# Optimization experiments

Hardware: AMD Instinct MI355X
Metric: run time of the kernel (lower is better)

## Reference

```python
import jax, jax.numpy as jnp
import numpy as np

B, LMAX, T_OUT, VOCAB, EMB, CVEC, HID, OUT = 8192, 12, 10, 36, 300, 256, 256, 512


def setup_inputs() -> dict:
    key = jax.random.key(0)
    ks = jax.random.split(key, 16)
    s = lambda fan: 1.0 / np.sqrt(fan)
    u = lambda k, shape, b: jax.random.uniform(k, shape, jnp.float32, -b, b)
    inp = {
        'words': jax.random.randint(ks[0], (B, LMAX), 0, VOCAB),
        'lengths': 1 + jax.random.randint(ks[1], (B,), 0, LMAX),  # in [1, LMAX]
        'emb_table': jax.random.normal(ks[2], (VOCAB, EMB), jnp.float32),
        'enc_w': u(ks[3], (CVEC, EMB), s(EMB)),
        'enc_b': u(ks[4], (CVEC,), s(EMB)),
        'wih_f': u(ks[5], (4 * HID, CVEC), s(HID)),
        'whh_f': u(ks[6], (4 * HID, HID), s(HID)),
        'bih_f': u(ks[7], (4 * HID,), s(HID)),
        'bhh_f': u(ks[8], (4 * HID,), s(HID)),
        'wih_b': u(ks[9], (4 * HID, CVEC), s(HID)),
        'whh_b': u(ks[10], (4 * HID, HID), s(HID)),
        'bih_b': u(ks[11], (4 * HID,), s(HID)),
        'bhh_b': u(ks[12], (4 * HID,), s(HID)),
        'out_w': u(ks[13], (OUT, 2 * HID), s(2 * HID)),
        'out_b': u(ks[14], (OUT,), s(2 * HID)),
    }
    return inp


def _interp_words(emb_table, words, lengths):
    # bilinear resize (L,300)->(10,300) with align_corners=True; width unchanged
    # so it is exact linear interpolation along the char axis.
    def one(word_row, L):
        Lf = (L - 1).astype(jnp.float32)
        pos = jnp.arange(T_OUT, dtype=jnp.float32) * Lf / (T_OUT - 1)  # (10,)
        i0 = jnp.floor(pos).astype(jnp.int32)
        i1 = jnp.minimum(i0 + 1, L - 1).astype(jnp.int32)
        f = (pos - i0.astype(jnp.float32))[:, None]
        e = emb_table[word_row]  # (LMAX, EMB)
        return e[i0] * (1.0 - f) + e[i1] * f  # (10, EMB)
    return jax.vmap(one)(words, lengths)  # (B, 10, EMB)


def _lstm(seq, wih, whh, bih, bhh):
    # seq: (T, B, In); PyTorch gate order i, f, g, o
    bsz = seq.shape[1]
    h0 = jnp.zeros((bsz, HID), seq.dtype)
    c0 = jnp.zeros((bsz, HID), seq.dtype)

    def step(carry, x_t):
        h, c = carry
        g = x_t @ wih.T + h @ whh.T + (bih + bhh)
        i, f, gg, o = jnp.split(g, 4, axis=-1)
        c = jax.nn.sigmoid(f) * c + jax.nn.sigmoid(i) * jnp.tanh(gg)
        h = jax.nn.sigmoid(o) * jnp.tanh(c)
        return (h, c), h

    _, hs = jax.lax.scan(step, (h0, c0), seq)
    return hs  # (T, B, HID)


def reference(words, lengths, emb_table, enc_w, enc_b, wih_f, whh_f, bih_f, bhh_f,
              wih_b, whh_b, bih_b, bhh_b, out_w, out_b):
    emb = _interp_words(emb_table, words, lengths)              # (B, 10, 300)
    cv = jax.nn.relu(emb @ enc_w.T + enc_b)                     # (B, 10, 256)
    seq = jnp.transpose(cv, (1, 0, 2))                          # (10, B, 256)
    h_f = _lstm(seq, wih_f, whh_f, bih_f, bhh_f)                # (10, B, 256)
    h_b = _lstm(seq[::-1], wih_b, whh_b, bih_b, bhh_b)[::-1]    # (10, B, 256)
    rec = jnp.concatenate([h_f, h_b], axis=-1)                  # (10, B, 512)
    out = rec @ out_w.T + out_b                                 # (10, B, 512)
    return jnp.transpose(out, (1, 0, 2))                        # (B, 10, 512)
```

## Files before the change

### kernel.cpp

```cpp
#include <hip/hip_runtime.h>
#include <hip/hip_fp16.h>

typedef _Float16 f16;
typedef _Float16 f16x8 __attribute__((ext_vector_type(8)));
typedef float    f32x4 __attribute__((ext_vector_type(4)));

#define NB   8192
#define TOUT 10
#define LMAX 12
#define EMB  300

__device__ __forceinline__ float sigm_(float x) {
    return __builtin_amdgcn_rcpf(1.0f + __builtin_amdgcn_exp2f(x * -1.44269504f));
}
__device__ __forceinline__ float tanh_(float x) {
    return 1.0f - 2.0f * __builtin_amdgcn_rcpf(1.0f + __builtin_amdgcn_exp2f(x * 2.88539008f));
}

__global__ __launch_bounds__(256) void pack_w2(
    const float* __restrict__ wih_f, const float* __restrict__ whh_f,
    const float* __restrict__ wih_b, const float* __restrict__ whh_b,
    f16* __restrict__ Wp) {
    int idx = blockIdx.x * 256 + threadIdx.x;
    int d   = idx >> 19;
    int r   = idx & 524287;
    int tile = r >> 9;
    int e    = r & 511;
    int kc = tile >> 6, nt = tile & 63;
    int khi = e >> 7, rem = e & 127, nl = rem >> 3, klo = rem & 7;
    int n = nt * 16 + nl;
    int k = kc * 32 + khi * 8 + klo;
    int w = n >> 7, rr = n & 127, gate = rr >> 5, u = w * 32 + (rr & 31);
    int srow = gate * 256 + u;
    const float* wih = d ? wih_b : wih_f;
    const float* whh = d ? whh_b : whh_f;
    float v = (k < 256) ? wih[srow * 256 + k] : whh[srow * 256 + (k - 256)];
    Wp[idx] = (f16)v;
}

__global__ __launch_bounds__(256) void pack_bias(
    const float* __restrict__ bih_f, const float* __restrict__ bhh_f,
    const float* __restrict__ bih_b, const float* __restrict__ bhh_b,
    float* __restrict__ bp) {
    int idx = blockIdx.x * 256 + threadIdx.x;
    int d = idx >> 10, n = idx & 1023;
    int w = n >> 7, rr = n & 127, gate = rr >> 5, u = w * 32 + (rr & 31);
    int srow = gate * 256 + u;
    bp[idx] = d ? (bih_b[srow] + bhh_b[srow]) : (bih_f[srow] + bhh_f[srow]);
}

__global__ __launch_bounds__(256) void pack_w3(
    const float* __restrict__ out_w, f16* __restrict__ W3p) {
    int idx = blockIdx.x * 256 + threadIdx.x;
    int tile = idx >> 9, e = idx & 511;
    int kc = tile >> 5, nt = tile & 31;
    int khi = e >> 7, rem = e & 127, nl = rem >> 3, klo = rem & 7;
    int n = nt * 16 + nl, k = kc * 32 + khi * 8 + klo;
    W3p[idx] = (f16)out_w[n * 512 + k];
}

__global__ __launch_bounds__(256) void enc_proj(
    const float* __restrict__ tab, const float* __restrict__ ew,
    const float* __restrict__ eb, float* __restrict__ P) {
    int v = blockIdx.x, j = threadIdx.x;
    const float* a = tab + v * EMB;
    const float* w = ew + j * EMB;
    float s = 0.0f;
    for (int k = 0; k < EMB; ++k) s += a[k] * w[k];
    P[v * 256 + j] = s + eb[j];
}

__global__ __launch_bounds__(256) void build_seq(
    const int* __restrict__ words, const int* __restrict__ lengths,
    const float* __restrict__ P, f16* __restrict__ seqp) {
    int gi = blockIdx.x * 256 + threadIdx.x;
    int bl  = gi & 15;
    int khi = (gi >> 4) & 3;
    int kc  = (gi >> 6) & 7;
    int mt  = (gi >> 9) & 511;
    int t   = gi >> 18;
    int b = mt * 16 + bl;
    int L = lengths[b];
    float pos = ((float)t * (float)(L - 1)) / 9.0f;
    int i0 = (int)pos;
    float f = pos - (float)i0;
    int i1 = min(i0 + 1, L - 1);
    int c0 = words[b * LMAX + i0];
    int c1 = words[b * LMAX + i1];
    const float* p0 = P + c0 * 256 + kc * 32 + khi * 8;
    const float* p1 = P + c1 * 256 + kc * 32 + khi * 8;
    f16x8 r;
#pragma unroll
    for (int j = 0; j < 8; ++j) {
        float v = p0[j] * (1.0f - f) + p1[j] * f;
        v = fmaxf(v, 0.0f);
        r[j] = (f16)v;
    }
    *((f16x8*)seqp + gi) = r;
}

__global__ __launch_bounds__(512) void lstm_fused(
    const f16* __restrict__ seqp, const f16* __restrict__ Wp,
    const float* __restrict__ bp, f16* __restrict__ hcat) {
    const int dir  = blockIdx.x >> 7;
    const int r0t  = (blockIdx.x & 127) << 2;
    const int wave = threadIdx.x >> 6;
    const int lane = threadIdx.x & 63;
    const int l16  = lane & 15;
    const int quad = lane >> 4;

    __shared__ __align__(16) f16 hbuf[4 * 8 * 512];

    {
        f16x8 z = {(f16)0, (f16)0, (f16)0, (f16)0, (f16)0, (f16)0, (f16)0, (f16)0};
        for (int i = threadIdx.x; i < 2048; i += 512) ((f16x8*)hbuf)[i] = z;
    }

    const float* bpd = bp + dir * 1024 + wave * 128;
    float bias_l[8];
#pragma unroll
    for (int nt = 0; nt < 8; ++nt) bias_l[nt] = bpd[nt * 16 + l16];

    const f16* Wd = Wp + dir * 524288;

    float cst[4][4][2];
#pragma unroll
    for (int m = 0; m < 4; ++m)
#pragma unroll
        for (int q = 0; q < 4; ++q) { cst[m][q][0] = 0.0f; cst[m][q][1] = 0.0f; }

    __syncthreads();

    for (int step = 0; step < TOUT; ++step) {
        const int t = dir ? (9 - step) : step;
        f32x4 acc[4][8];
#pragma unroll
        for (int m = 0; m < 4; ++m)
#pragma unroll
            for (int nt = 0; nt < 8; ++nt)
#pragma unroll
                for (int q = 0; q < 4; ++q) acc[m][nt][q] = bias_l[nt];

        const f16* seqt = seqp + (size_t)(t * 512 + r0t) * 8 * 512;

#pragma unroll 2
        for (int kc = 0; kc < 8; ++kc) {
            f16x8 bfrag[8];
#pragma unroll
            for (int nt = 0; nt < 8; ++nt)
                bfrag[nt] = *(const f16x8*)(Wd + ((kc * 64 + wave * 8 + nt) * 512 + lane * 8));
            f16x8 afrag[4];
#pragma unroll
            for (int m = 0; m < 4; ++m)
                afrag[m] = *(const f16x8*)(seqt + ((m * 8 + kc) * 512 + lane * 8));
#pragma unroll
            for (int m = 0; m < 4; ++m)
#pragma unroll
                for (int nt = 0; nt < 8; ++nt)
                    acc[m][nt] = __builtin_amdgcn_mfma_f32_16x16x32_f16(
                        afrag[m], bfrag[nt], acc[m][nt], 0, 0, 0);
        }
#pragma unroll 2
        for (int kcl = 0; kcl < 8; ++kcl) {
            int kc = kcl + 8;
            f16x8 bfrag[8];
#pragma unroll
            for (int nt = 0; nt < 8; ++nt)
                bfrag[nt] = *(const f16x8*)(Wd + ((kc * 64 + wave * 8 + nt) * 512 + lane * 8));
            f16x8 afrag[4];
#pragma unroll
            for (int m = 0; m < 4; ++m)
                afrag[m] = *(const f16x8*)(hbuf + ((m * 8 + kcl) * 512 + lane * 8));
#pragma unroll
            for (int m = 0; m < 4; ++m)
#pragma unroll
                for (int nt = 0; nt < 8; ++nt)
                    acc[m][nt] = __builtin_amdgcn_mfma_f32_16x16x32_f16(
                        afrag[m], bfrag[nt], acc[m][nt], 0, 0, 0);
        }

        __syncthreads();

#pragma unroll
        for (int m = 0; m < 4; ++m) {
#pragma unroll
            for (int us = 0; us < 2; ++us) {
#pragma unroll
                for (int q = 0; q < 4; ++q) {
                    float gi_ = acc[m][0 + us][q];
                    float gf_ = acc[m][2 + us][q];
                    float gg_ = acc[m][4 + us][q];
                    float go_ = acc[m][6 + us][q];
                    float ii = sigm_(gi_), ff = sigm_(gf_);
                    float gg = tanh_(gg_), oo = sigm_(go_);
                    float c = ff * cst[m][q][us] + ii * gg;
                    cst[m][q][us] = c;
                    float h = oo * tanh_(c);
                    int u   = us * 16 + l16;
                    int row = quad * 4 + q;
                    hbuf[(m * 8 + wave) * 512 + ((u >> 3) * 16 + row) * 8 + (u & 7)] = (f16)h;
                }
            }
        }

        __syncthreads();

        for (int i = threadIdx.x; i < 2048; i += 512) {
            int off = i * 8;
            int m  = off >> 12;
            int kc = (off >> 9) & 7;
            int e  = off & 511;
            f16x8 v = *(const f16x8*)(hbuf + off);
            *(f16x8*)(hcat + ((size_t)((t * 512 + r0t + m) * 16 + dir * 8 + kc) * 512 + e)) = v;
        }
    }
}

__global__ __launch_bounds__(512) void out_gemm(
    const f16* __restrict__ hcat, const f16* __restrict__ W3p,
    const float* __restrict__ out_b, float* __restrict__ out) {
    const int mt0  = blockIdx.x << 2;
    const int wave = threadIdx.x >> 6;
    const int lane = threadIdx.x & 63;
    const int l16  = lane & 15;
    const int quad = lane >> 4;
    const int n0   = wave * 64;

    float bias_l[4];
#pragma unroll
    for (int nt = 0; nt < 4; ++nt) bias_l[nt] = out_b[n0 + nt * 16 + l16];

    f32x4 acc[4][4];
#pragma unroll
    for (int m = 0; m < 4; ++m)
#pragma unroll
        for (int nt = 0; nt < 4; ++nt)
#pragma unroll
            for (int q = 0; q < 4; ++q) acc[m][nt][q] = bias_l[nt];

#pragma unroll 2
    for (int kc = 0; kc < 16; ++kc) {
        f16x8 a[4], b[4];
#pragma unroll
        for (int m = 0; m < 4; ++m)
            a[m] = *(const f16x8*)(hcat + ((size_t)((mt0 + m) * 16 + kc) * 512 + lane * 8));
#pragma unroll
        for (int nt = 0; nt < 4; ++nt)
            b[nt] = *(const f16x8*)(W3p + ((kc * 32 + wave * 4 + nt) * 512 + lane * 8));
#pragma unroll
        for (int m = 0; m < 4; ++m)
#pragma unroll
            for (int nt = 0; nt < 4; ++nt)
                acc[m][nt] = __builtin_amdgcn_mfma_f32_16x16x32_f16(a[m], b[nt], acc[m][nt], 0, 0, 0);
    }

#pragma unroll
    for (int m = 0; m < 4; ++m) {
#pragma unroll
        for (int nt = 0; nt < 4; ++nt) {
#pragma unroll
            for (int q = 0; q < 4; ++q) {
                int R = mt0 * 16 + m * 16 + quad * 4 + q;
                int t = R >> 13;
                int b = R & 8191;
                out[(size_t)(b * 10 + t) * 512 + n0 + nt * 16 + l16] = acc[m][nt][q];
            }
        }
    }
}

extern "C" void kernel_launch(void* const* d_in, const int* in_sizes, int n_in,
                              void* d_out, int out_size, void* d_ws, size_t ws_size,
                              hipStream_t stream) {
    const int*   words   = (const int*)d_in[0];
    const int*   lengths = (const int*)d_in[1];
    const float* tab     = (const float*)d_in[2];
    const float* enc_w   = (const float*)d_in[3];
    const float* enc_b   = (const float*)d_in[4];
    const float* wih_f   = (const float*)d_in[5];
    const float* whh_f   = (const float*)d_in[6];
    const float* bih_f   = (const float*)d_in[7];
    const float* bhh_f   = (const float*)d_in[8];
    const float* wih_b   = (const float*)d_in[9];
    const float* whh_b   = (const float*)d_in[10];
    const float* bih_b   = (const float*)d_in[11];
    const float* bhh_b   = (const float*)d_in[12];
    const float* out_w   = (const float*)d_in[13];
    const float* out_b   = (const float*)d_in[14];
    float* out = (float*)d_out;

    char* ws = (char*)d_ws;
    f16*   Wp   = (f16*)(ws + 0);
    f16*   W3p  = (f16*)(ws + 2097152);
    float* bp   = (float*)(ws + 2621440);
    float* P    = (float*)(ws + 2629632);
    f16*   seqp = (f16*)(ws + 2666496);
    f16*   hcat = (f16*)(ws + 44609536);

    pack_w2<<<4096, 256, 0, stream>>>(wih_f, whh_f, wih_b, whh_b, Wp);
    pack_bias<<<8, 256, 0, stream>>>(bih_f, bhh_f, bih_b, bhh_b, bp);
    pack_w3<<<1024, 256, 0, stream>>>(out_w, W3p);
    enc_proj<<<36, 256, 0, stream>>>(tab, enc_w, enc_b, P);
    build_seq<<<10240, 256, 0, stream>>>(words, lengths, P, seqp);
    lstm_fused<<<256, 512, 0, stream>>>(seqp, Wp, bp, hcat);
    out_gemm<<<1280, 512, 0, stream>>>(hcat, W3p, out_b, out);
}
```

Before: 488.3 us.

## Double-buffer LSTM hidden state, defer hcat store, pack h writes, widen out_gemm tile

The LSTM kernel now keeps the hidden state in two shared-memory buffers. This removes one barrier per step, and the previous step's h is written to global memory after the next step's MMA loop, so the store can overlap compute. The weight rows are permuted so each lane computes two adjacent units and stores them as one packed f16x2 value. The two k-loops are merged into one fully unrolled loop, and occupancy hints are added. out_gemm doubles its M tile to 8 so each W3 fragment is reused more, at the cost of more registers and half as many blocks.

```diff
diff --git a/kernel.cpp b/kernel.cpp
--- a/kernel.cpp
+++ b/kernel.cpp
@@ -2,6 +2,7 @@
 #include <hip/hip_fp16.h>
 
 typedef _Float16 f16;
+typedef _Float16 f16x2 __attribute__((ext_vector_type(2)));
 typedef _Float16 f16x8 __attribute__((ext_vector_type(8)));
 typedef float    f32x4 __attribute__((ext_vector_type(4)));
 
@@ -15,6 +16,10 @@
 }
 __device__ __forceinline__ float tanh_(float x) {
     return 1.0f - 2.0f * __builtin_amdgcn_rcpf(1.0f + __builtin_amdgcn_exp2f(x * 2.88539008f));
+}
+
+__device__ __forceinline__ f16x2 pk_f16(float a, float b) {
+    return __builtin_bit_cast(f16x2, __builtin_amdgcn_cvt_pkrtz(a, b));
 }
 
 __global__ __launch_bounds__(256) void pack_w2(
@@ -30,7 +35,8 @@
     int khi = e >> 7, rem = e & 127, nl = rem >> 3, klo = rem & 7;
     int n = nt * 16 + nl;
     int k = kc * 32 + khi * 8 + klo;
-    int w = n >> 7, rr = n & 127, gate = rr >> 5, u = w * 32 + (rr & 31);
+    int w = n >> 7, rr = n & 127, gate = rr >> 5;
+    int u = w * 32 + 2 * (rr & 15) + ((rr >> 4) & 1);
     int srow = gate * 256 + u;
     const float* wih = d ? wih_b : wih_f;
     const float* whh = d ? whh_b : whh_f;
@@ -44,7 +50,8 @@
     float* __restrict__ bp) {
     int idx = blockIdx.x * 256 + threadIdx.x;
     int d = idx >> 10, n = idx & 1023;
-    int w = n >> 7, rr = n & 127, gate = rr >> 5, u = w * 32 + (rr & 31);
+    int w = n >> 7, rr = n & 127, gate = rr >> 5;
+    int u = w * 32 + 2 * (rr & 15) + ((rr >> 4) & 1);
     int srow = gate * 256 + u;
     bp[idx] = d ? (bih_b[srow] + bhh_b[srow]) : (bih_f[srow] + bhh_f[srow]);
 }
@@ -99,7 +106,7 @@
     *((f16x8*)seqp + gi) = r;
 }
 
-__global__ __launch_bounds__(512) void lstm_fused(
+__global__ __launch_bounds__(512, 2) void lstm_fused(
     const f16* __restrict__ seqp, const f16* __restrict__ Wp,
     const float* __restrict__ bp, f16* __restrict__ hcat) {
     const int dir  = blockIdx.x >> 7;
@@ -109,11 +116,11 @@
     const int l16  = lane & 15;
     const int quad = lane >> 4;
 
-    __shared__ __align__(16) f16 hbuf[4 * 8 * 512];
+    __shared__ __align__(16) f16 hbuf[2][4 * 8 * 512];
 
     {
         f16x8 z = {(f16)0, (f16)0, (f16)0, (f16)0, (f16)0, (f16)0, (f16)0, (f16)0};
-        for (int i = threadIdx.x; i < 2048; i += 512) ((f16x8*)hbuf)[i] = z;
+        for (int i = threadIdx.x; i < 2048; i += 512) ((f16x8*)hbuf[0])[i] = z;
     }
 
     const float* bpd = bp + dir * 1024 + wave * 128;
@@ -123,6 +130,19 @@
 
     const f16* Wd = Wp + dir * 524288;
 
+    int   csrc[4];
+    size_t cdst[4];
+#pragma unroll
+    for (int r = 0; r < 4; ++r) {
+        int i = r * 512 + threadIdx.x;
+        int off = i * 8;
+        int m  = off >> 12;
+        int kc = (off >> 9) & 7;
+        int e  = off & 511;
+        csrc[r] = off;
+        cdst[r] = (size_t)(((r0t + m) * 16 + dir * 8 + kc) * 512 + e);
+    }
+
     float cst[4][4][2];
 #pragma unroll
     for (int m = 0; m < 4; ++m)
@@ -131,8 +151,12 @@
 
     __syncthreads();
 
+    int cur = 0;
     for (int step = 0; step < TOUT; ++step) {
         const int t = dir ? (9 - step) : step;
+        const f16* hb_r = hbuf[cur];
+        f16*       hb_w = hbuf[cur ^ 1];
+
         f32x4 acc[4][8];
 #pragma unroll
         for (int m = 0; m < 4; ++m)
@@ -141,18 +165,24 @@
 #pragma unroll
                 for (int q = 0; q < 4; ++q) acc[m][nt][q] = bias_l[nt];
 
-        const f16* seqt = seqp + (size_t)(t * 512 + r0t) * 8 * 512;
-
-#pragma unroll 2
-        for (int kc = 0; kc < 8; ++kc) {
+        const f16* seqt = seqp + (size_t)(t * 512 + r0t) * 4096;
+
+#pragma unroll
+        for (int kc = 0; kc < 16; ++kc) {
             f16x8 bfrag[8];
 #pragma unroll
             for (int nt = 0; nt < 8; ++nt)
                 bfrag[nt] = *(const f16x8*)(Wd + ((kc * 64 + wave * 8 + nt) * 512 + lane * 8));
             f16x8 afrag[4];
-#pragma unroll
-            for (int m = 0; m < 4; ++m)
-                afrag[m] = *(const f16x8*)(seqt + ((m * 8 + kc) * 512 + lane * 8));
+            if (kc < 8) {
+#pragma unroll
+                for (int m = 0; m < 4; ++m)
+                    afrag[m] = *(const f16x8*)(seqt + ((m * 8 + kc) * 512 + lane * 8));
+            } else {
+#pragma unroll
+                for (int m = 0; m < 4; ++m)
+                    afrag[m] = *(const f16x8*)(hb_r + ((m * 8 + (kc - 8)) * 512 + lane * 8));
+            }
 #pragma unroll
             for (int m = 0; m < 4; ++m)
 #pragma unroll
@@ -160,66 +190,53 @@
                     acc[m][nt] = __builtin_amdgcn_mfma_f32_16x16x32_f16(
                         afrag[m], bfrag[nt], acc[m][nt], 0, 0, 0);
         }
-#pragma unroll 2
-        for (int kcl = 0; kcl < 8; ++kcl) {
-            int kc = kcl + 8;
-            f16x8 bfrag[8];
-#pragma unroll
-            for (int nt = 0; nt < 8; ++nt)
-                bfrag[nt] = *(const f16x8*)(Wd + ((kc * 64 + wave * 8 + nt) * 512 + lane * 8));
-            f16x8 afrag[4];
-#pragma unroll
-            for (int m = 0; m < 4; ++m)
-                afrag[m] = *(const f16x8*)(hbuf + ((m * 8 + kcl) * 512 + lane * 8));
-#pragma unroll
-            for (int m = 0; m < 4; ++m)
-#pragma unroll
-                for (int nt = 0; nt < 8; ++nt)
-                    acc[m][nt] = __builtin_amdgcn_mfma_f32_16x16x32_f16(
-                        afrag[m], bfrag[nt], acc[m][nt], 0, 0, 0);
+
+        if (step > 0) {
+            const int tp = dir ? (t + 1) : (t - 1);
+            const size_t tb = (size_t)tp * 4194304;
+#pragma unroll
+            for (int r = 0; r < 4; ++r)
+                *(f16x8*)(hcat + tb + cdst[r]) = *(const f16x8*)(hb_r + csrc[r]);
         }
 
-        __syncthreads();
-
 #pragma unroll
         for (int m = 0; m < 4; ++m) {
 #pragma unroll
-            for (int us = 0; us < 2; ++us) {
-#pragma unroll
-                for (int q = 0; q < 4; ++q) {
-                    float gi_ = acc[m][0 + us][q];
-                    float gf_ = acc[m][2 + us][q];
-                    float gg_ = acc[m][4 + us][q];
-                    float go_ = acc[m][6 + us][q];
-                    float ii = sigm_(gi_), ff = sigm_(gf_);
-                    float gg = tanh_(gg_), oo = sigm_(go_);
-                    float c = ff * cst[m][q][us] + ii * gg;
-                    cst[m][q][us] = c;
-                    float h = oo * tanh_(c);
-                    int u   = us * 16 + l16;
-                    int row = quad * 4 + q;
-                    hbuf[(m * 8 + wave) * 512 + ((u >> 3) * 16 + row) * 8 + (u & 7)] = (f16)h;
-                }
+            for (int q = 0; q < 4; ++q) {
+                float i0 = acc[m][0][q], i1 = acc[m][1][q];
+                float f0 = acc[m][2][q], f1 = acc[m][3][q];
+                float g0 = acc[m][4][q], g1 = acc[m][5][q];
+                float o0 = acc[m][6][q], o1 = acc[m][7][q];
+                float c0 = sigm_(f0) * cst[m][q][0] + sigm_(i0) * tanh_(g0);
+                float c1 = sigm_(f1) * cst[m][q][1] + sigm_(i1) * tanh_(g1);
+                cst[m][q][0] = c0;
+                cst[m][q][1] = c1;
+                float h0 = sigm_(o0) * tanh_(c0);
+                float h1 = sigm_(o1) * tanh_(c1);
+                f16x2 hv = pk_f16(h0, h1);
+                *(f16x2*)&hb_w[(m * 8 + wave) * 512 +
+                               ((l16 >> 2) * 16 + quad * 4 + q) * 8 + 2 * (l16 & 3)] = hv;
             }
         }
 
         __syncthreads();
-
-        for (int i = threadIdx.x; i < 2048; i += 512) {
-            int off = i * 8;
-            int m  = off >> 12;
-            int kc = (off >> 9) & 7;
-            int e  = off & 511;
-            f16x8 v = *(const f16x8*)(hbuf + off);
-            *(f16x8*)(hcat + ((size_t)((t * 512 + r0t + m) * 16 + dir * 8 + kc) * 512 + e)) = v;
-        }
-    }
-}
-
-__global__ __launch_bounds__(512) void out_gemm(
+        cur ^= 1;
+    }
+
+    {
+        const int tl = dir ? 0 : 9;
+        const size_t tb = (size_t)tl * 4194304;
+        const f16* hb_r = hbuf[cur];
+#pragma unroll
+        for (int r = 0; r < 4; ++r)
+            *(f16x8*)(hcat + tb + cdst[r]) = *(const f16x8*)(hb_r + csrc[r]);
+    }
+}
+
+__global__ __launch_bounds__(512, 2) void out_gemm(
     const f16* __restrict__ hcat, const f16* __restrict__ W3p,
     const float* __restrict__ out_b, float* __restrict__ out) {
-    const int mt0  = blockIdx.x << 2;
+    const int mt0  = blockIdx.x << 3;
     const int wave = threadIdx.x >> 6;
     const int lane = threadIdx.x & 63;
     const int l16  = lane & 15;
@@ -230,37 +247,38 @@
 #pragma unroll
     for (int nt = 0; nt < 4; ++nt) bias_l[nt] = out_b[n0 + nt * 16 + l16];
 
-    f32x4 acc[4][4];
-#pragma unroll
-    for (int m = 0; m < 4; ++m)
+    f32x4 acc[8][4];
+#pragma unroll
+    for (int m = 0; m < 8; ++m)
 #pragma unroll
         for (int nt = 0; nt < 4; ++nt)
 #pragma unroll
             for (int q = 0; q < 4; ++q) acc[m][nt][q] = bias_l[nt];
 
-#pragma unroll 2
+#pragma unroll 4
     for (int kc = 0; kc < 16; ++kc) {
-        f16x8 a[4], b[4];
-#pragma unroll
-        for (int m = 0; m < 4; ++m)
-            a[m] = *(const f16x8*)(hcat + ((size_t)((mt0 + m) * 16 + kc) * 512 + lane * 8));
+        f16x8 b[4];
 #pragma unroll
         for (int nt = 0; nt < 4; ++nt)
             b[nt] = *(const f16x8*)(W3p + ((kc * 32 + wave * 4 + nt) * 512 + lane * 8));
-#pragma unroll
-        for (int m = 0; m < 4; ++m)
+        f16x8 a[8];
+#pragma unroll
+        for (int m = 0; m < 8; ++m)
+            a[m] = *(const f16x8*)(hcat + ((size_t)((mt0 + m) * 16 + kc) * 512 + lane * 8));
+#pragma unroll
+        for (int m = 0; m < 8; ++m)
 #pragma unroll
             for (int nt = 0; nt < 4; ++nt)
                 acc[m][nt] = __builtin_amdgcn_mfma_f32_16x16x32_f16(a[m], b[nt], acc[m][nt], 0, 0, 0);
     }
 
 #pragma unroll
-    for (int m = 0; m < 4; ++m) {
+    for (int m = 0; m < 8; ++m) {
 #pragma unroll
         for (int nt = 0; nt < 4; ++nt) {
 #pragma unroll
             for (int q = 0; q < 4; ++q) {
-                int R = mt0 * 16 + m * 16 + quad * 4 + q;
+                int R = (mt0 + m) * 16 + quad * 4 + q;
                 int t = R >> 13;
                 int b = R & 8191;
                 out[(size_t)(b * 10 + t) * 512 + n0 + nt * 16 + l16] = acc[m][nt][q];
@@ -303,5 +321,5 @@
     enc_proj<<<36, 256, 0, stream>>>(tab, enc_w, enc_b, P);
     build_seq<<<10240, 256, 0, stream>>>(words, lengths, P, seqp);
     lstm_fused<<<256, 512, 0, stream>>>(seqp, Wp, bp, hcat);
-    out_gemm<<<1280, 512, 0, stream>>>(hcat, W3p, out_b, out);
-}
+    out_gemm<<<640, 512, 0, stream>>>(hcat, W3p, out_b, out);
+}
```

Result: slower. 1.226 ms (+151.1%).
